# Kernel optimization log

Measured on AMD Instinct MI355X. Metric: run time of the kernel, lower is better.

Reference implementation:

```python
import jax, jax.numpy as jnp
import numpy as np
import math

IN_DIM = 3
N_LEVELS = 16
N_FEATS = 2
LOG2_HASHMAP = 19
BASE_RES = 16
DESIRED_RES = 2048
N_POINTS = 1048576
# first in_dim hash primes from the torch module; all fit in uint32
PRIMES = np.array([1, 2654435761, 805459861], dtype=np.uint32)


def _level_params():
    # faithful to the torch code: growth exponent divides by (base_resolution - 1)
    beta = math.exp((math.log(DESIRED_RES) - math.log(BASE_RES)) / (BASE_RES - 1))
    res = [math.floor(BASE_RES * beta ** i) for i in range(N_LEVELS)]
    hms = [min(r ** IN_DIM, 2 ** LOG2_HASHMAP) for r in res]
    return res, hms


def setup_inputs() -> dict:
    key = jax.random.key(0)
    kx, kt = jax.random.split(key)
    x = jax.random.uniform(kx, (N_POINTS, IN_DIM), dtype=jnp.float32)
    # kaiming_uniform(a=sqrt(5)) on [hashmap, n_feats] -> bound = sqrt(1/2)
    bound = math.sqrt(0.5)
    tables = jax.random.uniform(kt, (N_LEVELS, 2 ** LOG2_HASHMAP, N_FEATS),
                                dtype=jnp.float32, minval=-bound, maxval=bound)
    return {"x": x, "tables": tables}


def _forward(x, tables):
    res, hms = _level_params()
    neighbors = np.arange(1 << IN_DIM, dtype=np.int64).reshape(-1, 1)   # [8,1]
    dims = np.arange(IN_DIM, dtype=np.int64).reshape(1, -1)             # [1,3]
    bin_mask = jnp.asarray((neighbors & (1 << dims)) == 0)              # [8,3] bool
    primes = jnp.asarray(PRIMES)                                        # [3] uint32
    outs = [x]  # include_input=True
    for l in range(N_LEVELS):
        xs = x * jnp.float32(res[l])                    # [N,3]
        xi = jnp.floor(xs).astype(jnp.int32)            # torch .long() trunc; x>=0 so floor==trunc
        xf = xs - xi.astype(xs.dtype)                   # fractional part (no grad via xi)
        xi = xi[..., None, :]                           # [N,1,3]
        xf = xf[..., None, :]                           # [N,1,3]
        idx = jnp.where(bin_mask, xi, xi + 1).astype(jnp.uint32)         # [N,8,3]
        w = jnp.prod(jnp.where(bin_mask, 1.0 - xf, xf), axis=-1, keepdims=True)  # [N,8,1]
        # hash: (idx * prime) mod 2^32 (uint32 wraparound == int64 mul & 0xFFFFFFFF), xor-fold, mod size
        h = idx * primes                                # [N,8,3] uint32
        h = h[..., 0] ^ h[..., 1] ^ h[..., 2]           # [N,8]
        h = (h % jnp.uint32(hms[l])).astype(jnp.int32)
        emb = tables[l][h]                              # [N,8,F] gather
        outs.append(jnp.sum(emb * w, axis=-2))          # [N,F]
    return jnp.concatenate(outs, axis=-1)               # [N, 3 + 16*2]


def reference(x, tables):
    return _forward(x, tables)
```

## Files before the change

### kernel.cpp

```cpp
#include <hip/hip_runtime.h>
#include <math.h>
#include <stdint.h>

#define NPTS   1048576
#define NLEV   16
#define TPB    256
#define ROW    35
#define TBL_ENTRIES (1u << 19)

typedef float f4 __attribute__((ext_vector_type(4)));
typedef float f2 __attribute__((ext_vector_type(2)));

struct LevelParams {
    float    resf;
    uint32_t hm;
    uint32_t is_pow2;
    uint32_t pad;
    uint64_t magic;
};
struct LPAll { LevelParams lv[NLEV]; };

__device__ __forceinline__ void hash_calc(
    float xv0, float xv1, float xv2, const LevelParams& P,
    unsigned (&hi)[8], float (&w)[8])
{
    const float xs0 = xv0 * P.resf, xs1 = xv1 * P.resf, xs2 = xv2 * P.resf;
    const float f0 = floorf(xs0), f1 = floorf(xs1), f2v = floorf(xs2);
    const float t0 = xs0 - f0, t1 = xs1 - f1, t2 = xs2 - f2v;

    const unsigned a0 = (unsigned)(int)f0;
    const unsigned a1 = a0 + 1u;
    const unsigned b0 = (unsigned)(int)f1 * 2654435761u;
    const unsigned b1 = ((unsigned)(int)f1 + 1u) * 2654435761u;
    const unsigned c0 = (unsigned)(int)f2v * 805459861u;
    const unsigned c1 = ((unsigned)(int)f2v + 1u) * 805459861u;

    const float wa0 = 1.f - t0, wa1 = t0;
    const float wb0 = 1.f - t1, wb1 = t1;
    const float wc0 = 1.f - t2, wc1 = t2;

    const uint32_t hmv  = P.hm;
    const uint32_t mask = hmv - 1u;
    const uint64_t M    = P.magic;
    const bool     p2   = (P.is_pow2 != 0);

    #pragma unroll
    for (int n = 0; n < 8; ++n) {
        unsigned h = ((n & 1) ? a1 : a0)
                   ^ ((n & 2) ? b1 : b0)
                   ^ ((n & 4) ? c1 : c0);
        if (p2) {
            hi[n] = h & mask;
        } else {
            uint64_t low = M * (uint64_t)h;
            hi[n] = (uint32_t)(((__uint128_t)low * hmv) >> 64);
        }
        w[n] = (((n & 1) ? wa1 : wa0) * ((n & 2) ? wb1 : wb0))
               * ((n & 4) ? wc1 : wc0);
    }
}

__global__ __launch_bounds__(TPB)
void hashgrid_gather1(const float* __restrict__ xall,
                      const float* __restrict__ tb,
                      f2* __restrict__ wrow_all,
                      LevelParams P)
{
    const int tid = threadIdx.x;
    const int p0  = blockIdx.x * (TPB * 2);

    const f2*    tbl = (const f2*)tb;
    const float* xp  = xall + (size_t)p0 * 3;
    f2*          wrow = wrow_all + p0;

    const int piA = tid;
    const int piB = tid + TPB;

    const float xa0 = __builtin_nontemporal_load(&xp[piA * 3 + 0]);
    const float xa1 = __builtin_nontemporal_load(&xp[piA * 3 + 1]);
    const float xa2 = __builtin_nontemporal_load(&xp[piA * 3 + 2]);
    const float xb0 = __builtin_nontemporal_load(&xp[piB * 3 + 0]);
    const float xb1 = __builtin_nontemporal_load(&xp[piB * 3 + 1]);
    const float xb2 = __builtin_nontemporal_load(&xp[piB * 3 + 2]);

    unsigned hA[8]; float wA[8];
    unsigned hB[8]; float wB[8];
    hash_calc(xa0, xa1, xa2, P, hA, wA);
    hash_calc(xb0, xb1, xb2, P, hB, wB);

    f2 eA[8], eB[8];
    #pragma unroll
    for (int n = 0; n < 8; ++n) eA[n] = tbl[hA[n]];
    #pragma unroll
    for (int n = 0; n < 8; ++n) eB[n] = tbl[hB[n]];

    float accA0 = 0.f, accA1 = 0.f, accB0 = 0.f, accB1 = 0.f;
    #pragma unroll
    for (int n = 0; n < 8; ++n) {
        accA0 = fmaf(eA[n].x, wA[n], accA0);
        accA1 = fmaf(eA[n].y, wA[n], accA1);
    }
    #pragma unroll
    for (int n = 0; n < 8; ++n) {
        accB0 = fmaf(eB[n].x, wB[n], accB0);
        accB1 = fmaf(eB[n].y, wB[n], accB1);
    }

    f2 vA; vA.x = accA0; vA.y = accA1;
    f2 vB; vB.x = accB0; vB.y = accB1;
    __builtin_nontemporal_store(vA, &wrow[piA]);
    __builtin_nontemporal_store(vB, &wrow[piB]);
}

__global__ __launch_bounds__(TPB)
void hashgrid_interleave(const float* __restrict__ x,
                         const float* __restrict__ ws,
                         float* __restrict__ out)
{
    __shared__ float srow[TPB * ROW];
    const int tid = threadIdx.x;
    const int p0  = blockIdx.x * TPB;

    const float* xblk = x + (size_t)p0 * 3;
    #pragma unroll
    for (int j = 0; j < 3; ++j) {
        int idx = tid + j * TPB;
        int p = idx / 3, c = idx - p * 3;
        srow[p * ROW + c] = __builtin_nontemporal_load(&xblk[idx]);
    }
    const f2* wsv = (const f2*)ws;
    #pragma unroll
    for (int l = 0; l < NLEV; ++l) {
        f2 v = __builtin_nontemporal_load(&wsv[(size_t)l * NPTS + p0 + tid]);
        srow[tid * ROW + 3 + 2 * l] = v.x;
        srow[tid * ROW + 4 + 2 * l] = v.y;
    }
    __syncthreads();

    f4*       outv = (f4*)(out + (size_t)p0 * ROW);
    const f4* sv   = (const f4*)srow;
    for (int j = tid; j < (TPB * ROW) / 4; j += TPB)
        __builtin_nontemporal_store(sv[j], &outv[j]);
}

__global__ __launch_bounds__(TPB)
void hashgrid_lvl(const float* __restrict__ x,
                  const float* __restrict__ tables,
                  float* __restrict__ out,
                  LPAll lp, int base)
{
    const int tid = threadIdx.x;
    const int lvl = base + (blockIdx.x & 7);
    const int p0  = (blockIdx.x >> 3) * TPB;

    const float* xp = x + (size_t)p0 * 3;
    const float xv0 = xp[tid * 3 + 0];
    const float xv1 = xp[tid * 3 + 1];
    const float xv2 = xp[tid * 3 + 2];

    const LevelParams P   = lp.lv[lvl];
    const f2*         tbl = (const f2*)(tables + (size_t)lvl * TBL_ENTRIES * 2);

    unsigned hi[8]; float w[8];
    hash_calc(xv0, xv1, xv2, P, hi, w);
    float acc0 = 0.f, acc1 = 0.f;
    #pragma unroll
    for (int n = 0; n < 8; ++n) {
        f2 e = tbl[hi[n]];
        acc0 = fmaf(e.x, w[n], acc0);
        acc1 = fmaf(e.y, w[n], acc1);
    }

    float* orow = out + (size_t)(p0 + tid) * ROW;
    __builtin_nontemporal_store(acc0, &orow[3 + 2 * lvl]);
    __builtin_nontemporal_store(acc1, &orow[4 + 2 * lvl]);
    if (lvl == 0) {
        __builtin_nontemporal_store(xv0, &orow[0]);
        __builtin_nontemporal_store(xv1, &orow[1]);
        __builtin_nontemporal_store(xv2, &orow[2]);
    }
}

extern "C" void kernel_launch(void* const* d_in, const int* in_sizes, int n_in,
                              void* d_out, int out_size, void* d_ws, size_t ws_size,
                              hipStream_t stream)
{
    const float* x      = (const float*)d_in[0];
    const float* tables = (const float*)d_in[1];
    float*       out    = (float*)d_out;

    LPAll lp;
    const double beta = exp((log(2048.0) - log(16.0)) / 15.0);
    for (int i = 0; i < NLEV; ++i) {
        double r = floor(16.0 * pow(beta, (double)i));
        double h3 = r * r * r;
        uint32_t hm = (h3 < (double)(1u << 19)) ? (uint32_t)h3 : (1u << 19);
        lp.lv[i].resf    = (float)r;
        lp.lv[i].hm      = hm;
        lp.lv[i].is_pow2 = ((hm & (hm - 1u)) == 0u) ? 1u : 0u;
        lp.lv[i].pad     = 0;
        lp.lv[i].magic   = lp.lv[i].is_pow2 ? 0ull : (~0ull / hm + 1ull);
    }

    const size_t ws_need = (size_t)NLEV * NPTS * 2 * sizeof(float);
    if (ws_size >= ws_need) {
        const int gblocks = NPTS / (TPB * 2);
        for (int l = 0; l < NLEV; ++l) {
            hashgrid_gather1<<<gblocks, TPB, 0, stream>>>(
                x,
                tables + (size_t)l * TBL_ENTRIES * 2,
                (f2*)d_ws + (size_t)l * NPTS,
                lp.lv[l]);
        }
        hashgrid_interleave<<<NPTS / TPB, TPB, 0, stream>>>(x, (const float*)d_ws, out);
    } else {
        const int nblocks = 8 * (NPTS / TPB);
        hashgrid_lvl<<<nblocks, TPB, 0, stream>>>(x, tables, out, lp, 0);
        hashgrid_lvl<<<nblocks, TPB, 0, stream>>>(x, tables, out, lp, 8);
    }
}
```

Before: 438.6 us.

## Fuse the five coarsest hash levels into the final interleave kernel

Levels 0-4 are no longer computed by separate per-level gather kernels writing to workspace. They are computed directly inside the final interleave kernel, whose tables are small and likely cache-resident. This removes five kernel launches and their workspace write and read traffic. In exchange the final kernel does more gather and hash work per thread and may need more registers.

```diff
diff --git a/kernel.cpp b/kernel.cpp
--- a/kernel.cpp
+++ b/kernel.cpp
@@ -4,6 +4,7 @@
 
 #define NPTS   1048576
 #define NLEV   16
+#define NBIG   11
 #define TPB    256
 #define ROW    35
 #define TBL_ENTRIES (1u << 19)
@@ -113,27 +114,83 @@
 }
 
 __global__ __launch_bounds__(TPB)
-void hashgrid_interleave(const float* __restrict__ x,
-                         const float* __restrict__ ws,
-                         float* __restrict__ out)
+void hashgrid_final(const float* __restrict__ x,
+                    const float* __restrict__ tables,
+                    const float* __restrict__ ws,
+                    float* __restrict__ out,
+                    LPAll lp)
 {
     __shared__ float srow[TPB * ROW];
     const int tid = threadIdx.x;
     const int p0  = blockIdx.x * TPB;
-
-    const float* xblk = x + (size_t)p0 * 3;
-    #pragma unroll
-    for (int j = 0; j < 3; ++j) {
-        int idx = tid + j * TPB;
-        int p = idx / 3, c = idx - p * 3;
-        srow[p * ROW + c] = __builtin_nontemporal_load(&xblk[idx]);
-    }
+    const int pi  = p0 + tid;
+
+    const float xv0 = __builtin_nontemporal_load(&x[(size_t)pi * 3 + 0]);
+    const float xv1 = __builtin_nontemporal_load(&x[(size_t)pi * 3 + 1]);
+    const float xv2 = __builtin_nontemporal_load(&x[(size_t)pi * 3 + 2]);
+
+    srow[tid * ROW + 0] = xv0;
+    srow[tid * ROW + 1] = xv1;
+    srow[tid * ROW + 2] = xv2;
+
     const f2* wsv = (const f2*)ws;
     #pragma unroll
-    for (int l = 0; l < NLEV; ++l) {
-        f2 v = __builtin_nontemporal_load(&wsv[(size_t)l * NPTS + p0 + tid]);
+    for (int l = 5; l < NLEV; ++l) {
+        f2 v = __builtin_nontemporal_load(&wsv[(size_t)(l - 5) * NPTS + pi]);
         srow[tid * ROW + 3 + 2 * l] = v.x;
         srow[tid * ROW + 4 + 2 * l] = v.y;
+    }
+
+    #pragma unroll
+    for (int lp2 = 0; lp2 < 4; lp2 += 2) {
+        const LevelParams PA = lp.lv[lp2];
+        const LevelParams PB = lp.lv[lp2 + 1];
+        const f2* tA = (const f2*)(tables + (size_t)lp2 * TBL_ENTRIES * 2);
+        const f2* tB = (const f2*)(tables + (size_t)(lp2 + 1) * TBL_ENTRIES * 2);
+
+        unsigned hA[8]; float wA[8];
+        unsigned hB[8]; float wB[8];
+        hash_calc(xv0, xv1, xv2, PA, hA, wA);
+        hash_calc(xv0, xv1, xv2, PB, hB, wB);
+
+        f2 eA[8], eB[8];
+        #pragma unroll
+        for (int n = 0; n < 8; ++n) eA[n] = tA[hA[n]];
+        #pragma unroll
+        for (int n = 0; n < 8; ++n) eB[n] = tB[hB[n]];
+
+        float a0 = 0.f, a1 = 0.f, b0 = 0.f, b1 = 0.f;
+        #pragma unroll
+        for (int n = 0; n < 8; ++n) {
+            a0 = fmaf(eA[n].x, wA[n], a0);
+            a1 = fmaf(eA[n].y, wA[n], a1);
+        }
+        #pragma unroll
+        for (int n = 0; n < 8; ++n) {
+            b0 = fmaf(eB[n].x, wB[n], b0);
+            b1 = fmaf(eB[n].y, wB[n], b1);
+        }
+        srow[tid * ROW + 3 + 2 * lp2]     = a0;
+        srow[tid * ROW + 4 + 2 * lp2]     = a1;
+        srow[tid * ROW + 3 + 2 * (lp2+1)] = b0;
+        srow[tid * ROW + 4 + 2 * (lp2+1)] = b1;
+    }
+    {
+        const LevelParams P4 = lp.lv[4];
+        const f2* t4 = (const f2*)(tables + (size_t)4 * TBL_ENTRIES * 2);
+        unsigned h[8]; float w[8];
+        hash_calc(xv0, xv1, xv2, P4, h, w);
+        f2 e[8];
+        #pragma unroll
+        for (int n = 0; n < 8; ++n) e[n] = t4[h[n]];
+        float a0 = 0.f, a1 = 0.f;
+        #pragma unroll
+        for (int n = 0; n < 8; ++n) {
+            a0 = fmaf(e[n].x, w[n], a0);
+            a1 = fmaf(e[n].y, w[n], a1);
+        }
+        srow[tid * ROW + 3 + 8] = a0;
+        srow[tid * ROW + 4 + 8] = a1;
     }
     __syncthreads();
 
@@ -202,17 +259,18 @@
         lp.lv[i].magic   = lp.lv[i].is_pow2 ? 0ull : (~0ull / hm + 1ull);
     }
 
-    const size_t ws_need = (size_t)NLEV * NPTS * 2 * sizeof(float);
+    const size_t ws_need = (size_t)NBIG * NPTS * 2 * sizeof(float);
     if (ws_size >= ws_need) {
         const int gblocks = NPTS / (TPB * 2);
-        for (int l = 0; l < NLEV; ++l) {
+        for (int l = 5; l < NLEV; ++l) {
             hashgrid_gather1<<<gblocks, TPB, 0, stream>>>(
                 x,
                 tables + (size_t)l * TBL_ENTRIES * 2,
-                (f2*)d_ws + (size_t)l * NPTS,
+                (f2*)d_ws + (size_t)(l - 5) * NPTS,
                 lp.lv[l]);
         }
-        hashgrid_interleave<<<NPTS / TPB, TPB, 0, stream>>>(x, (const float*)d_ws, out);
+        hashgrid_final<<<NPTS / TPB, TPB, 0, stream>>>(
+            x, tables, (const float*)d_ws, out, lp);
     } else {
         const int nblocks = 8 * (NPTS / TPB);
         hashgrid_lvl<<<nblocks, TPB, 0, stream>>>(x, tables, out, lp, 0);
```

New measurement: 401.9 us. 1.09x faster.
